# Kernel tuning notes

Measured on AMD Instinct MI355X. Metric: run time of the kernel, lower is better.

## Reference

```python
import jax, jax.numpy as jnp
import numpy as np

N_NODES = 8   # module-layer pairs
N_EDGES = 32  # connections, 4 outgoing per node
B, H, W = 4, 1024, 1024
EXC_RATIO, EXC_VAL, INH_VAL = 0.8, 1.0, -0.5


def setup_inputs() -> dict:
    key = jax.random.key(0)
    k_sp, k_m, k_w = jax.random.split(key, 3)
    # binary spikes per source node: [N, B, H, W]
    spikes = (jax.random.uniform(k_sp, (N_NODES, B, H, W)) < 0.1).astype(jnp.float32)
    # excitatory/inhibitory mask per source node: [N, H, W]
    u = jax.random.uniform(k_m, (N_NODES, H, W))
    masks = jnp.where(u < EXC_RATIO, EXC_VAL, INH_VAL).astype(jnp.float32)
    # per-connection weight (randn * strength): [E, H, W]
    weights = jax.random.normal(k_w, (N_EDGES, H, W), dtype=jnp.float32) * 0.5
    # edge list: node i -> (i+1..i+4) mod N
    src_idx = jnp.repeat(jnp.arange(N_NODES), 4)
    dst_idx = (src_idx + jnp.tile(jnp.arange(1, 5), N_NODES)) % N_NODES
    return {"spikes": spikes, "masks": masks, "weights": weights,
            "src_idx": src_idx, "dst_idx": dst_idx}


def reference(spikes, masks, weights, src_idx, dst_idx):
    # per-edge signal: gather src spikes, modulate by src mask and edge weight
    # [E, B, H, W] = [E, B, H, W] * [E, 1, H, W] * [E, 1, H, W]
    sig = spikes[src_idx] * masks[src_idx][:, None] * weights[:, None]
    # scatter-sum into destination nodes: [N, B, H, W]
    out = jax.ops.segment_sum(sig, dst_idx, num_segments=spikes.shape[0])
    return out
```

## Files before the change

kernel.cpp:

```cpp
#include <hip/hip_runtime.h>


#define HW (1024 * 1024)
#define NN 8
#define NB 4

typedef float f32x2 __attribute__((ext_vector_type(2)));

__global__ __launch_bounds__(256, 4) void axon_kernel(
    const float* __restrict__ spikes,
    const float* __restrict__ masks,
    const float* __restrict__ weights,
    float* __restrict__ out)
{
    const int t = blockIdx.x * blockDim.x + threadIdx.x;
    const int p = t * 2;

    f32x2 acc[NN][NB];
#pragma unroll
    for (int n = 0; n < NN; ++n)
#pragma unroll
        for (int b = 0; b < NB; ++b) acc[n][b] = (f32x2)(0.0f);

#pragma unroll
    for (int src = 0; src < NN; ++src) {
        const f32x2 m = *reinterpret_cast<const f32x2*>(masks + src * HW + p);

        f32x2 s[NB];
#pragma unroll
        for (int b = 0; b < NB; ++b)
            s[b] = *reinterpret_cast<const f32x2*>(spikes + (src * NB + b) * HW + p);

#pragma unroll
        for (int b = 0; b < NB; ++b) s[b] *= m;

#pragma unroll
        for (int k = 0; k < 4; ++k) {
            const int e   = src * 4 + k;
            const int dst = (src + k + 1) & 7;
            const f32x2 w = *reinterpret_cast<const f32x2*>(weights + e * HW + p);
#pragma unroll
            for (int b = 0; b < NB; ++b) {
                acc[dst][b].x = fmaf(s[b].x, w.x, acc[dst][b].x);
                acc[dst][b].y = fmaf(s[b].y, w.y, acc[dst][b].y);
            }
        }
    }

#pragma unroll
    for (int n = 0; n < NN; ++n)
#pragma unroll
        for (int b = 0; b < NB; ++b)
            __builtin_nontemporal_store(
                acc[n][b], reinterpret_cast<f32x2*>(out + (n * NB + b) * HW + p));
}

extern "C" void kernel_launch(void* const* d_in, const int* in_sizes, int n_in,
                              void* d_out, int out_size, void* d_ws, size_t ws_size,
                              hipStream_t stream) {
    const float* spikes  = (const float*)d_in[0];
    const float* masks   = (const float*)d_in[1];
    const float* weights = (const float*)d_in[2];
    float* out = (float*)d_out;

    const int threads = 256;
    const int blocks  = (HW / 2) / threads;
    axon_kernel<<<blocks, threads, 0, stream>>>(spikes, masks, weights, out);
}
```

Baseline: 92.37 us.

## Widen to float4 per thread and process batch in two halves

Each thread now handles 4 contiguous pixels with 128-bit loads and stores instead of 2, halving the grid size. To keep register pressure bounded, the batch is split into two passes of two batch elements each. Each pass reloads masks and weights, so that traffic doubles in exchange for wider memory transactions and fewer threads. Weights and masks may be served from cache on the second pass, but there is a risk of extra DRAM traffic.

Measured after the change: 139.5 us. +51.1%, slower.

```diff
diff --git a/kernel.cpp b/kernel.cpp
--- a/kernel.cpp
+++ b/kernel.cpp
@@ -5,7 +5,7 @@
 #define NN 8
 #define NB 4
 
-typedef float f32x2 __attribute__((ext_vector_type(2)));
+typedef float f32x4 __attribute__((ext_vector_type(4)));
 
 __global__ __launch_bounds__(256, 4) void axon_kernel(
     const float* __restrict__ spikes,
@@ -14,45 +14,49 @@
     float* __restrict__ out)
 {
     const int t = blockIdx.x * blockDim.x + threadIdx.x;
-    const int p = t * 2;
-
-    f32x2 acc[NN][NB];
-#pragma unroll
-    for (int n = 0; n < NN; ++n)
-#pragma unroll
-        for (int b = 0; b < NB; ++b) acc[n][b] = (f32x2)(0.0f);
+    const int p = t * 4;
 
 #pragma unroll
-    for (int src = 0; src < NN; ++src) {
-        const f32x2 m = *reinterpret_cast<const f32x2*>(masks + src * HW + p);
+    for (int bp = 0; bp < 2; ++bp) {
+        const int b0 = 2 * bp;
 
-        f32x2 s[NB];
+        f32x4 acc[NN][2];
 #pragma unroll
-        for (int b = 0; b < NB; ++b)
-            s[b] = *reinterpret_cast<const f32x2*>(spikes + (src * NB + b) * HW + p);
+        for (int n = 0; n < NN; ++n) {
+            acc[n][0] = (f32x4)(0.0f);
+            acc[n][1] = (f32x4)(0.0f);
+        }
 
 #pragma unroll
-        for (int b = 0; b < NB; ++b) s[b] *= m;
+        for (int src = 0; src < NN; ++src) {
+            const f32x4 m = *reinterpret_cast<const f32x4*>(masks + src * HW + p);
+
+            f32x4 s0 = *reinterpret_cast<const f32x4*>(spikes + (src * NB + b0 + 0) * HW + p);
+            f32x4 s1 = *reinterpret_cast<const f32x4*>(spikes + (src * NB + b0 + 1) * HW + p);
+            s0 *= m;
+            s1 *= m;
 
 #pragma unroll
-        for (int k = 0; k < 4; ++k) {
-            const int e   = src * 4 + k;
-            const int dst = (src + k + 1) & 7;
-            const f32x2 w = *reinterpret_cast<const f32x2*>(weights + e * HW + p);
+            for (int k = 0; k < 4; ++k) {
+                const int e   = src * 4 + k;
+                const int dst = (src + k + 1) & 7;
+                const f32x4 w = *reinterpret_cast<const f32x4*>(weights + e * HW + p);
 #pragma unroll
-            for (int b = 0; b < NB; ++b) {
-                acc[dst][b].x = fmaf(s[b].x, w.x, acc[dst][b].x);
-                acc[dst][b].y = fmaf(s[b].y, w.y, acc[dst][b].y);
+                for (int c = 0; c < 4; ++c) {
+                    acc[dst][0][c] = fmaf(s0[c], w[c], acc[dst][0][c]);
+                    acc[dst][1][c] = fmaf(s1[c], w[c], acc[dst][1][c]);
+                }
             }
         }
-    }
 
 #pragma unroll
-    for (int n = 0; n < NN; ++n)
-#pragma unroll
-        for (int b = 0; b < NB; ++b)
+        for (int n = 0; n < NN; ++n) {
             __builtin_nontemporal_store(
-                acc[n][b], reinterpret_cast<f32x2*>(out + (n * NB + b) * HW + p));
+                acc[n][0], reinterpret_cast<f32x4*>(out + (n * NB + b0 + 0) * HW + p));
+            __builtin_nontemporal_store(
+                acc[n][1], reinterpret_cast<f32x4*>(out + (n * NB + b0 + 1) * HW + p));
+        }
+    }
 }
 
 extern "C" void kernel_launch(void* const* d_in, const int* in_sizes, int n_in,
@@ -64,6 +68,6 @@
     float* out = (float*)d_out;
 
     const int threads = 256;
-    const int blocks  = (HW / 2) / threads;
+    const int blocks  = (HW / 4) / threads;
     axon_kernel<<<blocks, threads, 0, stream>>>(spikes, masks, weights, out);
 }
```
